# Kernel optimization log

Hardware: AMD Instinct MI355X
Metric: run time of the kernel (lower is better)

Reference implementation:

```python
import jax, jax.numpy as jnp
import numpy as np

N, D_IN, D_H, D_A, K = 131072, 768, 128, 32, 64
BN_EPS = 1e-5

def setup_inputs() -> dict:
    key = jax.random.key(0)
    ks = jax.random.split(key, 16)
    def lin(k, fan_in, shape):
        return (jax.random.uniform(k, shape, jnp.float32, -1.0, 1.0) / np.sqrt(fan_in)).astype(jnp.float32)
    return {
        "input": jax.random.normal(ks[0], (1, N, D_IN), jnp.float32),
        # linear: Linear(768,128) + BN(128)
        "W1": lin(ks[1], D_IN, (D_IN, D_H)), "b1": lin(ks[2], D_IN, (D_H,)),
        "g1": jnp.ones((D_H,), jnp.float32), "be1": jnp.zeros((D_H,), jnp.float32),
        # attention: Linear(128,32) + BN(32) + Tanh + Linear(32,1)
        "Watt1": lin(ks[3], D_H, (D_H, D_A)), "batt1": lin(ks[4], D_H, (D_A,)),
        "g2": jnp.ones((D_A,), jnp.float32), "be2": jnp.zeros((D_A,), jnp.float32),
        "Watt2": lin(ks[5], D_A, (D_A, 1)), "batt2": lin(ks[6], D_A, (1,)),
        # Wa ModuleList: three Linear(128,32, bias=False)
        "Wq": lin(ks[7], D_H, (D_H, D_A)),
        "Wk": lin(ks[8], D_H, (D_H, D_A)),
        "Wv": lin(ks[9], D_H, (D_H, D_A)),
        # linear_z: Linear(32*k, 128)
        "Wz": lin(ks[10], D_A * K, (D_A * K, D_H)), "bz": lin(ks[11], D_A * K, (D_H,)),
        # fc: Linear(128, 1)
        "Wf": lin(ks[12], D_H, (D_H, 1)), "bf": lin(ks[13], D_H, (1,)),
    }

def reference(input, W1, b1, g1, be1, Watt1, batt1, g2, be2, Watt2, batt2,
              Wq, Wk, Wv, Wz, bz, Wf, bf):
    k = Wz.shape[0] // D_A  # static
    inv = 1.0 / jnp.sqrt(1.0 + BN_EPS)  # BN eval: running_mean=0, running_var=1
    x = input[0]  # [N, 768]
    x = jax.nn.relu((x @ W1 + b1) * (g1 * inv) + be1)  # [N, 128]
    h = jnp.tanh((x @ Watt1 + batt1) * (g2 * inv) + be2)  # [N, 32]
    A = jax.nn.softmax((h @ Watt2 + batt2)[:, 0], axis=0)  # [N]
    order = jnp.argsort(-A)           # descending sort indices
    A_sorted = A[order]
    zs = x[order[:k]] * jax.nn.softmax(A_sorted[:k])[:, None]  # [k, 128]
    zq, zk_, zv = zs @ Wq, zs @ Wk, zs @ Wv                    # [k, 32] each
    zw = jax.nn.softmax(zq @ zk_.T, axis=1) @ zv               # [k, 32]
    zw = jax.nn.relu(zw.reshape(1, -1) @ Wz + bz)              # [1, 128]
    return zw @ Wf + bf                                        # [1, 1]
```

## Files before the change

kernel.cpp:

```cpp
#include <hip/hip_runtime.h>


#define NN   131072
#define DIN  768
#define DH   128
#define DA   32

using f32x4  = __attribute__((ext_vector_type(4))) float;
using bf16x8 = __attribute__((ext_vector_type(8))) __bf16;

#define WS_S      0
#define WS_PZ8    524288
#define WS_HIST   557056
#define WS_MISC   573440
#define WS_CIDX   573504
#define WS_CS     575552
#define WS_ORDER  577600
#define WS_W      577856
#define WS_ZQ     578112
#define WS_ZK     586304
#define WS_ZV     594496
#define WS_ZW     602688
#define WS_W1T    610944

__device__ __forceinline__ int s_bin(float s) {
  int b = (int)((s + 6.0f) * (4096.0f / 12.0f));
  return b < 0 ? 0 : (b > 4095 ? 4095 : b);
}

__device__ __forceinline__ void gl_lds16(const void* g, void* l) {
  __builtin_amdgcn_global_load_lds(
      (const __attribute__((address_space(1))) void*)g,
      (__attribute__((address_space(3))) void*)l, 16, 0, 0);
}

__global__ void k_prep(const float* __restrict__ W1, char* __restrict__ ws) {
  int T = blockIdx.x * 256 + threadIdx.x;
  if (T < 4112) ((int*)(ws + WS_HIST))[T] = 0;
  int u = T & 7, col = (T >> 3) & 127, kc = T >> 10;
  bf16x8 ov;
  #pragma unroll
  for (int j = 0; j < 8; ++j) {
    int k = (u & 3) * 8 + j;
    float v = W1[(size_t)(kc * 32 + k) * 128 + col];
    __bf16 h = (__bf16)v;
    ov[j] = (u < 4) ? h : (__bf16)(v - (float)h);
  }
  *(bf16x8*)(ws + WS_W1T + (size_t)kc * 16384 + col * 128 + ((u ^ (col & 7)) << 4)) = ov;
}

__global__ __launch_bounds__(256, 4) void k_main(
    const float* __restrict__ inp,
    const float* __restrict__ b1, const float* __restrict__ g1, const float* __restrict__ be1,
    const float* __restrict__ Watt1, const float* __restrict__ batt1,
    const float* __restrict__ g2, const float* __restrict__ be2,
    const float* __restrict__ Watt2, const float* __restrict__ batt2,
    char* __restrict__ ws)
{
  __shared__ __align__(16) char lds[32768];
  float* s_out = (float*)(ws + WS_S);
  float* pz8   = (float*)(ws + WS_PZ8);
  int*   hist  = (int*)(ws + WS_HIST);
  const char* w1t = ws + WS_W1T;

  const int t = threadIdx.x;
  const int l = t & 63;
  const int wid = t >> 6;
  const int r15 = l & 15, kg = l >> 4;
  const int blockRow = blockIdx.x * 64;
  const float inv = 1.0f / sqrtf(1.0f + 1e-5f);

  char* Bb0 = lds;
  char* Bb1 = lds + 16384;

  const float* aRow = inp + (size_t)(blockRow + wid * 16 + r15) * DIN + kg * 8;
  const int swzHi = (kg ^ (l & 7)) << 4;
  const int swzLo = ((4 | kg) ^ (l & 7)) << 4;

  f32x4 acc[8];
  #pragma unroll
  for (int i = 0; i < 8; ++i)
    #pragma unroll
    for (int q = 0; q < 4; ++q) acc[i][q] = 0.0f;

#define BDMA(Bbuf, kc_) do { \
    const char* s_ = w1t + (size_t)(kc_) * 16384 + t * 16; \
    char* d_ = (Bbuf) + t * 16; \
    gl_lds16(s_, d_); gl_lds16(s_ + 4096, d_ + 4096); \
    gl_lds16(s_ + 8192, d_ + 8192); gl_lds16(s_ + 12288, d_ + 12288); \
  } while (0)

#define ITER(Bcur, Bnxt, c0, c1, n0, n1, kc_) do { \
    if ((kc_) < 23) { \
      BDMA(Bnxt, (kc_) + 1); \
      const float* ap_ = aRow + ((kc_) + 1) * 32; \
      n0 = *(const f32x4*)ap_; n1 = *(const f32x4*)(ap_ + 4); \
      asm volatile("s_waitcnt vmcnt(6)" ::: "memory"); \
    } else { \
      asm volatile("s_waitcnt vmcnt(0)" ::: "memory"); \
    } \
    __builtin_amdgcn_sched_barrier(0); \
    __builtin_amdgcn_s_barrier(); \
    __builtin_amdgcn_sched_barrier(0); \
    bf16x8 ahi, alo; \
    _Pragma("unroll") \
    for (int j2 = 0; j2 < 4; ++j2) { \
      float x0 = c0[j2]; __bf16 h0 = (__bf16)x0; \
      ahi[j2] = h0; alo[j2] = (__bf16)(x0 - (float)h0); \
      float x1 = c1[j2]; __bf16 h1 = (__bf16)x1; \
      ahi[4 + j2] = h1; alo[4 + j2] = (__bf16)(x1 - (float)h1); \
    } \
    _Pragma("unroll") \
    for (int ni = 0; ni < 8; ++ni) { \
      const char* cb_ = (Bcur) + r15 * 128 + ni * 2048; \
      bf16x8 bhi = *(const bf16x8*)(cb_ + swzHi); \
      bf16x8 blo = *(const bf16x8*)(cb_ + swzLo); \
      acc[ni] = __builtin_amdgcn_mfma_f32_16x16x32_bf16(ahi, bhi, acc[ni], 0, 0, 0); \
      acc[ni] = __builtin_amdgcn_mfma_f32_16x16x32_bf16(ahi, blo, acc[ni], 0, 0, 0); \
      acc[ni] = __builtin_amdgcn_mfma_f32_16x16x32_bf16(alo, bhi, acc[ni], 0, 0, 0); \
    } \
    __builtin_amdgcn_sched_barrier(0); \
    __builtin_amdgcn_s_barrier(); \
    __builtin_amdgcn_sched_barrier(0); \
  } while (0)

  f32x4 pa0, pa1, pb0, pb1;
  BDMA(Bb0, 0);
  { const float* ap_ = aRow; pa0 = *(const f32x4*)ap_; pa1 = *(const f32x4*)(ap_ + 4); }

  for (int kc = 0; kc < 24; kc += 2) {
    ITER(Bb0, Bb1, pa0, pa1, pb0, pb1, kc);
    ITER(Bb1, Bb0, pb0, pb1, pa0, pa1, kc + 1);
  }
#undef ITER
#undef BDMA

  #pragma unroll
  for (int ni = 0; ni < 8; ++ni) {
    int col = ni * 16 + r15;
    float b1c = b1[col], s1c = g1[col] * inv, be1c = be1[col];
    #pragma unroll
    for (int q = 0; q < 4; ++q) {
      int row = wid * 16 + kg * 4 + q;
      float xv = fmaxf((acc[ni][q] + b1c) * s1c + be1c, 0.0f);
      *(float*)(lds + row * 512 + ((col * 4) ^ ((row & 31) << 4))) = xv;
    }
  }
  __syncthreads();

  {
    const int row = t >> 2, q4 = t & 3;
    const int rsw = (row & 31) << 4;
    float hacc[8];
    #pragma unroll
    for (int a = 0; a < 8; ++a) hacc[a] = 0.0f;
    const char* xrow = lds + row * 512;
    const float* watt = Watt1 + q4 * 8;
    for (int cb = 0; cb < 128; cb += 4) {
      f32x4 xv = *(const f32x4*)(xrow + ((cb * 4) ^ rsw));
      #pragma unroll
      for (int u = 0; u < 4; ++u) {
        const float* wrow = watt + (cb + u) * 32;
        f32x4 w0 = *(const f32x4*)(wrow);
        f32x4 w1 = *(const f32x4*)(wrow + 4);
        float xs = xv[u];
        #pragma unroll
        for (int q = 0; q < 4; ++q) {
          hacc[q]     += xs * w0[q];
          hacc[4 + q] += xs * w1[q];
        }
      }
    }
    float partial = 0.0f;
    #pragma unroll
    for (int a = 0; a < 8; ++a) {
      int ai = q4 * 8 + a;
      float hv = tanhf((hacc[a] + batt1[ai]) * (g2[ai] * inv) + be2[ai]);
      partial += hv * Watt2[ai];
    }
    partial += __shfl_xor(partial, 1, 64);
    partial += __shfl_xor(partial, 2, 64);
    float ev = 0.0f;
    if (q4 == 0) {
      float sv = partial + batt2[0];
      s_out[blockRow + row] = sv;
      atomicAdd(&hist[s_bin(sv)], 1);
      ev = expf(sv);
    }
    #pragma unroll
    for (int off = 32; off >= 1; off >>= 1) ev += __shfl_xor(ev, off, 64);
    if (l == 0) pz8[blockIdx.x * 4 + wid] = ev;
  }
}

__global__ void k_reduce(char* __restrict__ ws) {
  float* pz8 = (float*)(ws + WS_PZ8);
  int* hist = (int*)(ws + WS_HIST);
  float* miscf = (float*)(ws + WS_MISC);
  int* misci = (int*)(ws + WS_MISC);
  const int t = threadIdx.x;
  __shared__ float red[256];
  __shared__ int csum[256];
  float z = 0.0f;
  for (int i = t; i < 8192; i += 256) z += pz8[i];
  red[t] = z;
  int c = 0;
  #pragma unroll
  for (int u = 0; u < 16; ++u) c += hist[t * 16 + u];
  csum[t] = c;
  __syncthreads();
  for (int off = 128; off >= 1; off >>= 1) {
    if (t < off) red[t] += red[t + off];
    __syncthreads();
  }
  if (t == 0) {
    miscf[0] = red[0];
    int cum = 0, bstar = 0;
    for (int ch = 255; ch >= 0; --ch) {
      if (cum + csum[ch] >= 64) {
        for (int b = ch * 16 + 15; b >= ch * 16; --b) {
          cum += hist[b];
          if (cum >= 64) { bstar = b; break; }
        }
        break;
      }
      cum += csum[ch];
    }
    misci[3] = bstar;
    misci[2] = 0;
  }
}

__global__ void k_gather(char* __restrict__ ws) {
  const int i = blockIdx.x * 256 + threadIdx.x;
  float* s_out = (float*)(ws + WS_S);
  int* misci = (int*)(ws + WS_MISC);
  int* cidx = (int*)(ws + WS_CIDX);
  float* cs = (float*)(ws + WS_CS);
  float s = s_out[i];
  if (s_bin(s) >= misci[3]) {
    int pos = atomicAdd(&misci[2], 1);
    if (pos < 512) { cidx[pos] = i; cs[pos] = s; }
  }
}

__global__ void k_select(char* __restrict__ ws) {
  const int t = threadIdx.x;
  float* s_out = (float*)(ws + WS_S);
  int* misci = (int*)(ws + WS_MISC);
  float* miscf = (float*)(ws + WS_MISC);
  int* cidx = (int*)(ws + WS_CIDX);
  float* cs = (float*)(ws + WS_CS);
  int* order = (int*)(ws + WS_ORDER);
  float* wsel = (float*)(ws + WS_W);
  __shared__ unsigned long long keys[512];
  __shared__ float aLds[64];
  int cnt = misci[2]; if (cnt > 512) cnt = 512;
  for (int i = t; i < 512; i += 256) {
    unsigned long long kkey = 0xFFFFFFFFFFFFFFFFull;
    if (i < cnt) {
      unsigned u = __float_as_uint(cs[i]);
      u = (u & 0x80000000u) ? ~u : (u | 0x80000000u);
      unsigned du = ~u;
      kkey = ((unsigned long long)du << 32) | (unsigned)cidx[i];
    }
    keys[i] = kkey;
  }
  __syncthreads();
  for (int k = 2; k <= 512; k <<= 1) {
    for (int j = k >> 1; j > 0; j >>= 1) {
      for (int i = t; i < 512; i += 256) {
        int ixj = i ^ j;
        if (ixj > i) {
          bool up = ((i & k) == 0);
          unsigned long long a = keys[i], b2 = keys[ixj];
          if (up ? (a > b2) : (a < b2)) { keys[i] = b2; keys[ixj] = a; }
        }
      }
      __syncthreads();
    }
  }
  float Z = miscf[0];
  if (t < 64) {
    int idx = (int)(keys[t] & 0xFFFFFFFFull);
    order[t] = idx;
    aLds[t] = expf(s_out[idx]) / Z;
  }
  __syncthreads();
  if (t < 64) {
    float m = aLds[0];
    float e = expf(aLds[t] - m);
    float sum = e;
    #pragma unroll
    for (int off = 32; off >= 1; off >>= 1) sum += __shfl_xor(sum, off, 64);
    wsel[t] = e / sum;
  }
}

__global__ void k_zs(const float* __restrict__ inp, const float* __restrict__ W1,
                     const float* __restrict__ b1, const float* __restrict__ g1, const float* __restrict__ be1,
                     const float* __restrict__ Wq, const float* __restrict__ Wk, const float* __restrict__ Wv,
                     char* __restrict__ ws)
{
  const int t = threadIdx.x, b = blockIdx.x;
  int* order = (int*)(ws + WS_ORDER);
  float* wsel = (float*)(ws + WS_W);
  float* zq = (float*)(ws + WS_ZQ);
  float* zk = (float*)(ws + WS_ZK);
  float* zv = (float*)(ws + WS_ZV);
  __shared__ float rowS[768];
  __shared__ float zsS[128];
  const float inv = 1.0f / sqrtf(1.0f + 1e-5f);
  int r = order[b];
  float wgt = wsel[b];
  for (int i = t; i < 768; i += 256) rowS[i] = inp[(size_t)r * 768 + i];
  __syncthreads();
  if (t < 128) {
    float d = 0.0f;
    for (int k = 0; k < 768; ++k) d += rowS[k] * W1[(size_t)k * 128 + t];
    float x = fmaxf((d + b1[t]) * (g1[t] * inv) + be1[t], 0.0f);
    zsS[t] = x * wgt;
  }
  __syncthreads();
  if (t < 96) {
    int which = t >> 5, a = t & 31;
    const float* W = (which == 0) ? Wq : ((which == 1) ? Wk : Wv);
    float d = 0.0f;
    for (int c = 0; c < 128; ++c) d += zsS[c] * W[c * 32 + a];
    float* dst = (which == 0) ? zq : ((which == 1) ? zk : zv);
    dst[b * 32 + a] = d;
  }
}

__global__ void k_attn(char* __restrict__ ws, float* __restrict__ out) {
  const int t = threadIdx.x;
  if (t == 0) out[0] = 0.0f;
  float* zq = (float*)(ws + WS_ZQ);
  float* zk = (float*)(ws + WS_ZK);
  float* zv = (float*)(ws + WS_ZV);
  float* zw = (float*)(ws + WS_ZW);
  __shared__ float q[2048], kk[2048], v[2048], P[4096];
  for (int i = t; i < 2048; i += 256) { q[i] = zq[i]; kk[i] = zk[i]; v[i] = zv[i]; }
  __syncthreads();
  for (int o = t; o < 4096; o += 256) {
    int i = o >> 6, j = o & 63;
    float d = 0.0f;
    for (int a = 0; a < 32; ++a) d += q[i * 32 + a] * kk[j * 32 + a];
    P[o] = d;
  }
  __syncthreads();
  if (t < 64) {
    float m = -1e30f;
    for (int j = 0; j < 64; ++j) m = fmaxf(m, P[t * 64 + j]);
    float sum = 0.0f;
    for (int j = 0; j < 64; ++j) { float e = expf(P[t * 64 + j] - m); P[t * 64 + j] = e; sum += e; }
    float rs = 1.0f / sum;
    for (int j = 0; j < 64; ++j) P[t * 64 + j] *= rs;
  }
  __syncthreads();
  for (int o = t; o < 2048; o += 256) {
    int i = o >> 5, a = o & 31;
    float d = 0.0f;
    for (int j = 0; j < 64; ++j) d += P[i * 64 + j] * v[j * 32 + a];
    zw[o] = d;
  }
}

__global__ void k_wz(const float* __restrict__ Wz, const float* __restrict__ bz,
                     const float* __restrict__ Wf, const float* __restrict__ bf_,
                     char* __restrict__ ws, float* __restrict__ out) {
  const int t = threadIdx.x, j = blockIdx.x;
  float* zw = (float*)(ws + WS_ZW);
  __shared__ float red[256];
  float p = 0.0f;
  for (int i2 = t; i2 < 2048; i2 += 256) p += zw[i2] * Wz[(size_t)i2 * 128 + j];
  red[t] = p; __syncthreads();
  for (int off = 128; off >= 1; off >>= 1) {
    if (t < off) red[t] += red[t + off];
    __syncthreads();
  }
  if (t == 0) {
    float o = fmaxf(red[0] + bz[j], 0.0f);
    float contrib = o * Wf[j] + (j == 0 ? bf_[0] : 0.0f);
    atomicAdd(out, contrib);
  }
}

extern "C" void kernel_launch(void* const* d_in, const int* in_sizes, int n_in,
                              void* d_out, int out_size, void* d_ws, size_t ws_size,
                              hipStream_t stream) {
  const float* inp   = (const float*)d_in[0];
  const float* W1    = (const float*)d_in[1];
  const float* b1    = (const float*)d_in[2];
  const float* g1    = (const float*)d_in[3];
  const float* be1   = (const float*)d_in[4];
  const float* Watt1 = (const float*)d_in[5];
  const float* batt1 = (const float*)d_in[6];
  const float* g2    = (const float*)d_in[7];
  const float* be2   = (const float*)d_in[8];
  const float* Watt2 = (const float*)d_in[9];
  const float* batt2 = (const float*)d_in[10];
  const float* Wq    = (const float*)d_in[11];
  const float* Wk    = (const float*)d_in[12];
  const float* Wv    = (const float*)d_in[13];
  const float* Wz    = (const float*)d_in[14];
  const float* bz    = (const float*)d_in[15];
  const float* Wf    = (const float*)d_in[16];
  const float* bf_   = (const float*)d_in[17];
  char* ws = (char*)d_ws;

  k_prep<<<dim3(96), dim3(256), 0, stream>>>(W1, ws);
  k_main<<<dim3(2048), dim3(256), 0, stream>>>(inp, b1, g1, be1, Watt1, batt1, g2, be2, Watt2, batt2, ws);
  k_reduce<<<dim3(1), dim3(256), 0, stream>>>(ws);
  k_gather<<<dim3(512), dim3(256), 0, stream>>>(ws);
  k_select<<<dim3(1), dim3(256), 0, stream>>>(ws);
  k_zs<<<dim3(64), dim3(256), 0, stream>>>(inp, W1, b1, g1, be1, Wq, Wk, Wv, ws);
  k_attn<<<dim3(1), dim3(256), 0, stream>>>(ws, (float*)d_out);
  k_wz<<<dim3(128), dim3(256), 0, stream>>>(Wz, bz, Wf, bf_, ws, (float*)d_out);
}
```

Measured before the change: 324.8 us.

## Stage A tiles through LDS with coalesced loads and triple-buffered B pipeline

Replaces per-lane strided A loads with coalesced 16-byte row loads held in registers and staged into swizzled LDS, and moves the W1 B tiles to a three-deep LDS ring so DMA for chunk kc+2 overlaps compute on kc. A larger LDS footprint (72KB) and a launch bound of two blocks per SM accompany it, with hand-tuned vmcnt waits per iteration. This trades occupancy and register pressure for deeper prefetch and better global load coalescing on the input stream.

```diff
diff --git a/kernel.cpp b/kernel.cpp
--- a/kernel.cpp
+++ b/kernel.cpp
@@ -49,7 +49,7 @@
   *(bf16x8*)(ws + WS_W1T + (size_t)kc * 16384 + col * 128 + ((u ^ (col & 7)) << 4)) = ov;
 }
 
-__global__ __launch_bounds__(256, 4) void k_main(
+__global__ __launch_bounds__(256, 2) void k_main(
     const float* __restrict__ inp,
     const float* __restrict__ b1, const float* __restrict__ g1, const float* __restrict__ be1,
     const float* __restrict__ Watt1, const float* __restrict__ batt1,
@@ -57,7 +57,7 @@
     const float* __restrict__ Watt2, const float* __restrict__ batt2,
     char* __restrict__ ws)
 {
-  __shared__ __align__(16) char lds[32768];
+  __shared__ __align__(16) char lds[73728];
   float* s_out = (float*)(ws + WS_S);
   float* pz8   = (float*)(ws + WS_PZ8);
   int*   hist  = (int*)(ws + WS_HIST);
@@ -67,74 +67,107 @@
   const int l = t & 63;
   const int wid = t >> 6;
   const int r15 = l & 15, kg = l >> 4;
+  const int l31 = l & 31, lrow2 = l >> 5, l7 = l & 7;
   const int blockRow = blockIdx.x * 64;
   const float inv = 1.0f / sqrtf(1.0f + 1e-5f);
 
-  char* Bb0 = lds;
-  char* Bb1 = lds + 16384;
-
-  const float* aRow = inp + (size_t)(blockRow + wid * 16 + r15) * DIN + kg * 8;
-  const int swzHi = (kg ^ (l & 7)) << 4;
-  const int swzLo = ((4 | kg) ^ (l & 7)) << 4;
-
+  const float* aBase = inp + (size_t)(blockRow + wid * 16 + lrow2) * DIN + l31 * 4;
+  const int swzHi = (kg ^ l7) << 4;
+  const int swzLo = ((4 | kg) ^ l7) << 4;
+
+  f32x4 a_st[2][8][2];
   f32x4 acc[8];
   #pragma unroll
   for (int i = 0; i < 8; ++i)
     #pragma unroll
     for (int q = 0; q < 4; ++q) acc[i][q] = 0.0f;
 
-#define BDMA(Bbuf, kc_) do { \
+#define APIECE(cb, c_, q_) do { \
+    const float* r0 = aBase + (size_t)(2*(q_)) * DIN + (c_) * 256; \
+    const float* r1 = aBase + (size_t)(2*(q_)+1) * DIN + (c_) * 256; \
+    a_st[cb][2*(q_)][0]   = *(const f32x4*)(r0); \
+    a_st[cb][2*(q_)][1]   = *(const f32x4*)(r0 + 128); \
+    a_st[cb][2*(q_)+1][0] = *(const f32x4*)(r1); \
+    a_st[cb][2*(q_)+1][1] = *(const f32x4*)(r1 + 128); \
+  } while (0)
+
+#define AWRITE(cb, s_) do { \
+    const int cc_ = (s_) & 7, h_ = cc_ >> 2, q_ = cc_ & 3; \
+    if ((l31 >> 3) == q_) { \
+      char* sb = lds + ((s_) % 3) * 8192; \
+      _Pragma("unroll") \
+      for (int rp = 0; rp < 8; ++rp) { \
+        int row = (wid << 4) + (rp << 1) + lrow2; \
+        *(f32x4*)(sb + row * 128 + ((l7 ^ (row & 7)) << 4)) = a_st[cb][rp][h_]; \
+      } \
+    } \
+  } while (0)
+
+#define BDMA(kc_) do { \
     const char* s_ = w1t + (size_t)(kc_) * 16384 + t * 16; \
-    char* d_ = (Bbuf) + t * 16; \
+    char* d_ = lds + 24576 + ((kc_) % 3) * 16384 + t * 16; \
     gl_lds16(s_, d_); gl_lds16(s_ + 4096, d_ + 4096); \
     gl_lds16(s_ + 8192, d_ + 8192); gl_lds16(s_ + 12288, d_ + 12288); \
   } while (0)
 
-#define ITER(Bcur, Bnxt, c0, c1, n0, n1, kc_) do { \
-    if ((kc_) < 23) { \
-      BDMA(Bnxt, (kc_) + 1); \
-      const float* ap_ = aRow + ((kc_) + 1) * 32; \
-      n0 = *(const f32x4*)ap_; n1 = *(const f32x4*)(ap_ + 4); \
-      asm volatile("s_waitcnt vmcnt(6)" ::: "memory"); \
-    } else { \
-      asm volatile("s_waitcnt vmcnt(0)" ::: "memory"); \
-    } \
-    __builtin_amdgcn_sched_barrier(0); \
-    __builtin_amdgcn_s_barrier(); \
-    __builtin_amdgcn_sched_barrier(0); \
+#define WAITN(n) asm volatile("s_waitcnt vmcnt(" #n ") lgkmcnt(0)" ::: "memory")
+
+#define COMP(kc_) do { \
+    const char* arow = lds + ((kc_) % 3) * 8192 + (wid * 16 + r15) * 128; \
+    const int rs_ = r15 & 7; \
+    f32x4 a0 = *(const f32x4*)(arow + (((2 * kg)     ^ rs_) << 4)); \
+    f32x4 a1 = *(const f32x4*)(arow + (((2 * kg + 1) ^ rs_) << 4)); \
     bf16x8 ahi, alo; \
     _Pragma("unroll") \
     for (int j2 = 0; j2 < 4; ++j2) { \
-      float x0 = c0[j2]; __bf16 h0 = (__bf16)x0; \
+      float x0 = a0[j2]; __bf16 h0 = (__bf16)x0; \
       ahi[j2] = h0; alo[j2] = (__bf16)(x0 - (float)h0); \
-      float x1 = c1[j2]; __bf16 h1 = (__bf16)x1; \
+      float x1 = a1[j2]; __bf16 h1 = (__bf16)x1; \
       ahi[4 + j2] = h1; alo[4 + j2] = (__bf16)(x1 - (float)h1); \
     } \
+    const char* bbuf = lds + 24576 + ((kc_) % 3) * 16384; \
     _Pragma("unroll") \
     for (int ni = 0; ni < 8; ++ni) { \
-      const char* cb_ = (Bcur) + r15 * 128 + ni * 2048; \
+      const char* cb_ = bbuf + r15 * 128 + ni * 2048; \
       bf16x8 bhi = *(const bf16x8*)(cb_ + swzHi); \
       bf16x8 blo = *(const bf16x8*)(cb_ + swzLo); \
       acc[ni] = __builtin_amdgcn_mfma_f32_16x16x32_bf16(ahi, bhi, acc[ni], 0, 0, 0); \
       acc[ni] = __builtin_amdgcn_mfma_f32_16x16x32_bf16(ahi, blo, acc[ni], 0, 0, 0); \
       acc[ni] = __builtin_amdgcn_mfma_f32_16x16x32_bf16(alo, bhi, acc[ni], 0, 0, 0); \
     } \
-    __builtin_amdgcn_sched_barrier(0); \
-    __builtin_amdgcn_s_barrier(); \
-    __builtin_amdgcn_sched_barrier(0); \
   } while (0)
 
-  f32x4 pa0, pa1, pb0, pb1;
-  BDMA(Bb0, 0);
-  { const float* ap_ = aRow; pa0 = *(const f32x4*)ap_; pa1 = *(const f32x4*)(ap_ + 4); }
-
-  for (int kc = 0; kc < 24; kc += 2) {
-    ITER(Bb0, Bb1, pa0, pa1, pb0, pb1, kc);
-    ITER(Bb1, Bb0, pb0, pb1, pa0, pa1, kc + 1);
-  }
-#undef ITER
+  #pragma unroll
+  for (int q = 0; q < 4; ++q) APIECE(0, 0, q);
+  BDMA(0); BDMA(1);
+  AWRITE(0, 0);
+  asm volatile("s_waitcnt lgkmcnt(0)" ::: "memory");
+  __builtin_amdgcn_s_barrier();
+  __builtin_amdgcn_sched_barrier(0);
+
+  #pragma unroll
+  for (int kc = 0; kc < 24; ++kc) {
+    if (kc <= 11 && (kc & 7) < 4) APIECE(((kc >> 3) + 1) & 1, (kc >> 3) + 1, kc & 7);
+    if (kc <= 22) AWRITE(((kc + 1) >> 3) & 1, kc + 1);
+    if      (kc == 0)                                    WAITN(8);
+    else if (kc == 1 || kc == 2 || kc == 3 ||
+             kc == 9 || kc == 10 || kc == 11)            WAITN(12);
+    else if (kc == 4 || kc == 8 || kc == 12)             WAITN(8);
+    else if (kc == 23)                                   WAITN(0);
+    else                                                 WAITN(4);
+    __builtin_amdgcn_sched_barrier(0);
+    __builtin_amdgcn_s_barrier();
+    __builtin_amdgcn_sched_barrier(0);
+    if (kc <= 21) BDMA(kc + 2);
+    COMP(kc);
+  }
+#undef COMP
+#undef WAITN
 #undef BDMA
-
+#undef AWRITE
+#undef APIECE
+
+  __syncthreads();
   #pragma unroll
   for (int ni = 0; ni < 8; ++ni) {
     int col = ni * 16 + r15;
```

New measurement: 347.4 us. 1.07x slower.

## Use single-pass bf16 GEMM with exact fp32 rescoring of top-k candidates

Applied to the files above, without the earlier changes.

Replaces the three-MFMA split-bf16 (hi/lo) emulation of the fp32 first GEMM with a single bf16 MFMA pass. B fragments now load straight from global memory into registers with a 4-deep A prefetch, instead of LDS DMA with double buffering. The x tile is stored in bf16 in LDS, and the candidate histogram threshold is widened by 24 bins to absorb the precision loss. A new kernel recomputes exact fp32 scores for every candidate so that selection and ordering stay correct. The aim is to cut MFMA work and LDS traffic, at the cost of an extra launch and a risk that the approximate softmax normaliser Z and the candidate window miss near-ties.

```diff
diff --git a/kernel.cpp b/kernel.cpp
--- a/kernel.cpp
+++ b/kernel.cpp
@@ -28,28 +28,18 @@
   return b < 0 ? 0 : (b > 4095 ? 4095 : b);
 }
 
-__device__ __forceinline__ void gl_lds16(const void* g, void* l) {
-  __builtin_amdgcn_global_load_lds(
-      (const __attribute__((address_space(1))) void*)g,
-      (__attribute__((address_space(3))) void*)l, 16, 0, 0);
-}
-
 __global__ void k_prep(const float* __restrict__ W1, char* __restrict__ ws) {
   int T = blockIdx.x * 256 + threadIdx.x;
   if (T < 4112) ((int*)(ws + WS_HIST))[T] = 0;
-  int u = T & 7, col = (T >> 3) & 127, kc = T >> 10;
+  int kg = T & 3, col = (T >> 2) & 127, kc = T >> 9;
   bf16x8 ov;
   #pragma unroll
-  for (int j = 0; j < 8; ++j) {
-    int k = (u & 3) * 8 + j;
-    float v = W1[(size_t)(kc * 32 + k) * 128 + col];
-    __bf16 h = (__bf16)v;
-    ov[j] = (u < 4) ? h : (__bf16)(v - (float)h);
-  }
-  *(bf16x8*)(ws + WS_W1T + (size_t)kc * 16384 + col * 128 + ((u ^ (col & 7)) << 4)) = ov;
-}
-
-__global__ __launch_bounds__(256, 4) void k_main(
+  for (int j = 0; j < 8; ++j)
+    ov[j] = (__bf16)W1[(size_t)(kc * 32 + kg * 8 + j) * 128 + col];
+  *(bf16x8*)(ws + WS_W1T + (size_t)kc * 8192 + col * 64 + kg * 16) = ov;
+}
+
+__global__ __launch_bounds__(256, 3) void k_main(
     const float* __restrict__ inp,
     const float* __restrict__ b1, const float* __restrict__ g1, const float* __restrict__ be1,
     const float* __restrict__ Watt1, const float* __restrict__ batt1,
@@ -57,7 +47,7 @@
     const float* __restrict__ Watt2, const float* __restrict__ batt2,
     char* __restrict__ ws)
 {
-  __shared__ __align__(16) char lds[32768];
+  __shared__ __align__(16) char lds[16384];
   float* s_out = (float*)(ws + WS_S);
   float* pz8   = (float*)(ws + WS_PZ8);
   int*   hist  = (int*)(ws + WS_HIST);
@@ -70,12 +60,8 @@
   const int blockRow = blockIdx.x * 64;
   const float inv = 1.0f / sqrtf(1.0f + 1e-5f);
 
-  char* Bb0 = lds;
-  char* Bb1 = lds + 16384;
-
-  const float* aRow = inp + (size_t)(blockRow + wid * 16 + r15) * DIN + kg * 8;
-  const int swzHi = (kg ^ (l & 7)) << 4;
-  const int swzLo = ((4 | kg) ^ (l & 7)) << 4;
+  const float* aP = inp + (size_t)(blockRow + wid * 16 + r15) * DIN + kg * 8;
+  const char* bP = w1t + r15 * 64 + kg * 16;
 
   f32x4 acc[8];
   #pragma unroll
@@ -83,57 +69,55 @@
     #pragma unroll
     for (int q = 0; q < 4; ++q) acc[i][q] = 0.0f;
 
-#define BDMA(Bbuf, kc_) do { \
-    const char* s_ = w1t + (size_t)(kc_) * 16384 + t * 16; \
-    char* d_ = (Bbuf) + t * 16; \
-    gl_lds16(s_, d_); gl_lds16(s_ + 4096, d_ + 4096); \
-    gl_lds16(s_ + 8192, d_ + 8192); gl_lds16(s_ + 12288, d_ + 12288); \
+#define LOADB(s, kc_) do { const char* bb_ = bP + (size_t)(kc_) * 8192; \
+    s##0 = *(const bf16x8*)(bb_);          s##1 = *(const bf16x8*)(bb_ + 1024); \
+    s##2 = *(const bf16x8*)(bb_ + 2048);   s##3 = *(const bf16x8*)(bb_ + 3072); \
+    s##4 = *(const bf16x8*)(bb_ + 4096);   s##5 = *(const bf16x8*)(bb_ + 5120); \
+    s##6 = *(const bf16x8*)(bb_ + 6144);   s##7 = *(const bf16x8*)(bb_ + 7168); \
   } while (0)
-
-#define ITER(Bcur, Bnxt, c0, c1, n0, n1, kc_) do { \
-    if ((kc_) < 23) { \
-      BDMA(Bnxt, (kc_) + 1); \
-      const float* ap_ = aRow + ((kc_) + 1) * 32; \
-      n0 = *(const f32x4*)ap_; n1 = *(const f32x4*)(ap_ + 4); \
-      asm volatile("s_waitcnt vmcnt(6)" ::: "memory"); \
-    } else { \
-      asm volatile("s_waitcnt vmcnt(0)" ::: "memory"); \
+#define LOADA(x0, x1, kc_) do { const float* ap_ = aP + (kc_) * 32; \
+    x0 = *(const f32x4*)(ap_); x1 = *(const f32x4*)(ap_ + 4); } while (0)
+#define BODY(pa0, pa1, bs, bn, kcb, kca) do { \
+    bf16x8 ah_; \
+    _Pragma("unroll") \
+    for (int j_ = 0; j_ < 4; ++j_) { \
+      ah_[j_]     = (__bf16)pa0[j_]; \
+      ah_[4 + j_] = (__bf16)pa1[j_]; \
     } \
-    __builtin_amdgcn_sched_barrier(0); \
-    __builtin_amdgcn_s_barrier(); \
-    __builtin_amdgcn_sched_barrier(0); \
-    bf16x8 ahi, alo; \
-    _Pragma("unroll") \
-    for (int j2 = 0; j2 < 4; ++j2) { \
-      float x0 = c0[j2]; __bf16 h0 = (__bf16)x0; \
-      ahi[j2] = h0; alo[j2] = (__bf16)(x0 - (float)h0); \
-      float x1 = c1[j2]; __bf16 h1 = (__bf16)x1; \
-      ahi[4 + j2] = h1; alo[4 + j2] = (__bf16)(x1 - (float)h1); \
-    } \
-    _Pragma("unroll") \
-    for (int ni = 0; ni < 8; ++ni) { \
-      const char* cb_ = (Bcur) + r15 * 128 + ni * 2048; \
-      bf16x8 bhi = *(const bf16x8*)(cb_ + swzHi); \
-      bf16x8 blo = *(const bf16x8*)(cb_ + swzLo); \
-      acc[ni] = __builtin_amdgcn_mfma_f32_16x16x32_bf16(ahi, bhi, acc[ni], 0, 0, 0); \
-      acc[ni] = __builtin_amdgcn_mfma_f32_16x16x32_bf16(ahi, blo, acc[ni], 0, 0, 0); \
-      acc[ni] = __builtin_amdgcn_mfma_f32_16x16x32_bf16(alo, bhi, acc[ni], 0, 0, 0); \
-    } \
-    __builtin_amdgcn_sched_barrier(0); \
-    __builtin_amdgcn_s_barrier(); \
-    __builtin_amdgcn_sched_barrier(0); \
+    LOADB(bn, kcb); \
+    LOADA(pa0, pa1, kca); \
+    acc[0] = __builtin_amdgcn_mfma_f32_16x16x32_bf16(ah_, bs##0, acc[0], 0, 0, 0); \
+    acc[1] = __builtin_amdgcn_mfma_f32_16x16x32_bf16(ah_, bs##1, acc[1], 0, 0, 0); \
+    acc[2] = __builtin_amdgcn_mfma_f32_16x16x32_bf16(ah_, bs##2, acc[2], 0, 0, 0); \
+    acc[3] = __builtin_amdgcn_mfma_f32_16x16x32_bf16(ah_, bs##3, acc[3], 0, 0, 0); \
+    acc[4] = __builtin_amdgcn_mfma_f32_16x16x32_bf16(ah_, bs##4, acc[4], 0, 0, 0); \
+    acc[5] = __builtin_amdgcn_mfma_f32_16x16x32_bf16(ah_, bs##5, acc[5], 0, 0, 0); \
+    acc[6] = __builtin_amdgcn_mfma_f32_16x16x32_bf16(ah_, bs##6, acc[6], 0, 0, 0); \
+    acc[7] = __builtin_amdgcn_mfma_f32_16x16x32_bf16(ah_, bs##7, acc[7], 0, 0, 0); \
   } while (0)
 
-  f32x4 pa0, pa1, pb0, pb1;
-  BDMA(Bb0, 0);
-  { const float* ap_ = aRow; pa0 = *(const f32x4*)ap_; pa1 = *(const f32x4*)(ap_ + 4); }
-
-  for (int kc = 0; kc < 24; kc += 2) {
-    ITER(Bb0, Bb1, pa0, pa1, pb0, pb1, kc);
-    ITER(Bb1, Bb0, pb0, pb1, pa0, pa1, kc + 1);
-  }
-#undef ITER
-#undef BDMA
+  f32x4 q00, q01, q10, q11, q20, q21, q30, q31;
+  bf16x8 bc0, bc1, bc2, bc3, bc4, bc5, bc6, bc7;
+  bf16x8 bn0, bn1, bn2, bn3, bn4, bn5, bn6, bn7;
+  LOADA(q00, q01, 0); LOADA(q10, q11, 1); LOADA(q20, q21, 2); LOADA(q30, q31, 3);
+  LOADB(bc, 0);
+
+  #pragma unroll 1
+  for (int kc4 = 0; kc4 < 6; ++kc4) {
+    const int kc = kc4 * 4;
+    const int p4 = (kc + 4 < 24) ? kc + 4 : 23;
+    const int p5 = (kc + 5 < 24) ? kc + 5 : 23;
+    const int p6 = (kc + 6 < 24) ? kc + 6 : 23;
+    const int p7 = (kc + 7 < 24) ? kc + 7 : 23;
+    const int b4 = (kc + 4 < 24) ? kc + 4 : 23;
+    BODY(q00, q01, bc, bn, kc + 1, p4);
+    BODY(q10, q11, bn, bc, kc + 2, p5);
+    BODY(q20, q21, bc, bn, kc + 3, p6);
+    BODY(q30, q31, bn, bc, b4,     p7);
+  }
+#undef BODY
+#undef LOADA
+#undef LOADB
 
   #pragma unroll
   for (int ni = 0; ni < 8; ++ni) {
@@ -143,27 +127,27 @@
     for (int q = 0; q < 4; ++q) {
       int row = wid * 16 + kg * 4 + q;
       float xv = fmaxf((acc[ni][q] + b1c) * s1c + be1c, 0.0f);
-      *(float*)(lds + row * 512 + ((col * 4) ^ ((row & 31) << 4))) = xv;
+      *(__bf16*)(lds + row * 256 + (((col >> 3) ^ (row & 15)) << 4) + (col & 7) * 2) =
+          (__bf16)xv;
     }
   }
   __syncthreads();
 
   {
     const int row = t >> 2, q4 = t & 3;
-    const int rsw = (row & 31) << 4;
     float hacc[8];
     #pragma unroll
     for (int a = 0; a < 8; ++a) hacc[a] = 0.0f;
-    const char* xrow = lds + row * 512;
-    const float* watt = Watt1 + q4 * 8;
-    for (int cb = 0; cb < 128; cb += 4) {
-      f32x4 xv = *(const f32x4*)(xrow + ((cb * 4) ^ rsw));
+    const char* xrow = lds + row * 256;
+    const int rsw = row & 15;
+    for (int ub = 0; ub < 16; ++ub) {
+      bf16x8 xv = *(const bf16x8*)(xrow + (((ub) ^ rsw) << 4));
       #pragma unroll
-      for (int u = 0; u < 4; ++u) {
-        const float* wrow = watt + (cb + u) * 32;
+      for (int j = 0; j < 8; ++j) {
+        const float* wrow = Watt1 + (ub * 8 + j) * 32 + q4 * 8;
         f32x4 w0 = *(const f32x4*)(wrow);
         f32x4 w1 = *(const f32x4*)(wrow + 4);
-        float xs = xv[u];
+        float xs = (float)xv[j];
         #pragma unroll
         for (int q = 0; q < 4; ++q) {
           hacc[q]     += xs * w0[q];
@@ -226,7 +210,7 @@
       }
       cum += csum[ch];
     }
-    misci[3] = bstar;
+    misci[3] = (bstar > 24) ? bstar - 24 : 0;
     misci[2] = 0;
   }
 }
@@ -244,9 +228,48 @@
   }
 }
 
+__global__ void k_exact(const float* __restrict__ inp, const float* __restrict__ W1,
+                        const float* __restrict__ b1, const float* __restrict__ g1,
+                        const float* __restrict__ be1,
+                        const float* __restrict__ Watt1, const float* __restrict__ batt1,
+                        const float* __restrict__ g2, const float* __restrict__ be2,
+                        const float* __restrict__ Watt2, const float* __restrict__ batt2,
+                        char* __restrict__ ws)
+{
+  int* misci = (int*)(ws + WS_MISC);
+  int* cidx = (int*)(ws + WS_CIDX);
+  float* cs = (float*)(ws + WS_CS);
+  const int b = blockIdx.x, t = threadIdx.x;
+  int cnt = misci[2]; if (cnt > 512) cnt = 512;
+  if (b >= cnt) return;
+  __shared__ float rowS[768];
+  __shared__ float xS[128];
+  __shared__ float hS[32];
+  const float inv = 1.0f / sqrtf(1.0f + 1e-5f);
+  const int r = cidx[b];
+  for (int i = t; i < 768; i += 256) rowS[i] = inp[(size_t)r * 768 + i];
+  __syncthreads();
+  if (t < 128) {
+    float d = 0.0f;
+    for (int k = 0; k < 768; ++k) d += rowS[k] * W1[(size_t)k * 128 + t];
+    xS[t] = fmaxf((d + b1[t]) * (g1[t] * inv) + be1[t], 0.0f);
+  }
+  __syncthreads();
+  if (t < 32) {
+    float d = 0.0f;
+    for (int c = 0; c < 128; ++c) d += xS[c] * Watt1[c * 32 + t];
+    hS[t] = tanhf((d + batt1[t]) * (g2[t] * inv) + be2[t]);
+  }
+  __syncthreads();
+  if (t == 0) {
+    float s = 0.0f;
+    for (int a = 0; a < 32; ++a) s += hS[a] * Watt2[a];
+    cs[b] = s + batt2[0];
+  }
+}
+
 __global__ void k_select(char* __restrict__ ws) {
   const int t = threadIdx.x;
-  float* s_out = (float*)(ws + WS_S);
   int* misci = (int*)(ws + WS_MISC);
   float* miscf = (float*)(ws + WS_MISC);
   int* cidx = (int*)(ws + WS_CIDX);
@@ -282,9 +305,12 @@
   }
   float Z = miscf[0];
   if (t < 64) {
-    int idx = (int)(keys[t] & 0xFFFFFFFFull);
-    order[t] = idx;
-    aLds[t] = expf(s_out[idx]) / Z;
+    unsigned du = (unsigned)(keys[t] >> 32);
+    unsigned m = ~du;
+    float sx = (m & 0x80000000u) ? __uint_as_float(m & 0x7fffffffu)
+                                 : __uint_as_float(~m);
+    order[t] = (int)(keys[t] & 0xFFFFFFFFull);
+    aLds[t] = expf(sx) / Z;
   }
   __syncthreads();
   if (t < 64) {
@@ -409,10 +435,11 @@
   const float* bf_   = (const float*)d_in[17];
   char* ws = (char*)d_ws;
 
-  k_prep<<<dim3(96), dim3(256), 0, stream>>>(W1, ws);
+  k_prep<<<dim3(48), dim3(256), 0, stream>>>(W1, ws);
   k_main<<<dim3(2048), dim3(256), 0, stream>>>(inp, b1, g1, be1, Watt1, batt1, g2, be2, Watt2, batt2, ws);
   k_reduce<<<dim3(1), dim3(256), 0, stream>>>(ws);
   k_gather<<<dim3(512), dim3(256), 0, stream>>>(ws);
+  k_exact<<<dim3(512), dim3(256), 0, stream>>>(inp, W1, b1, g1, be1, Watt1, batt1, g2, be2, Watt2, batt2, ws);
   k_select<<<dim3(1), dim3(256), 0, stream>>>(ws);
   k_zs<<<dim3(64), dim3(256), 0, stream>>>(inp, W1, b1, g1, be1, Wq, Wk, Wv, ws);
   k_attn<<<dim3(1), dim3(256), 0, stream>>>(ws, (float*)d_out);
```

Result: slower. 388.6 us (+19.7%).
